# Kernel optimization log

Hardware: AMD Instinct MI355X
Metric: run time of the kernel (lower is better)

Reference implementation:

```python
import jax, jax.numpy as jnp
import numpy as np

B, N, D = 2048, 16384, 16
SIGMA0 = 0.1
LOG2PI = float(np.log(2.0 * np.pi))


def setup_inputs() -> dict:
    key = jax.random.key(0)
    k1, k2 = jax.random.split(key)
    x = jax.random.normal(k1, (B, D), dtype=jnp.float32)
    mu = jax.random.normal(k2, (N, D), dtype=jnp.float32)
    # from_sigma == log (to_sigma == exp): sigmatilde = log(sigma0)
    sigmatilde = jnp.full((N,), np.log(SIGMA0), dtype=jnp.float32)
    weights = jnp.full((N,), 1.0 / N, dtype=jnp.float32)
    return {"x": x, "mu": mu, "sigmatilde": sigmatilde, "weights": weights}


def reference(x, mu, sigmatilde, weights):
    # sigma per kernel, shape [N]
    sigma = jnp.exp(sigmatilde)
    # squared euclidean distance ||x - mu||^2 via gemm form, shape [B, N]
    sq = (
        jnp.sum(x * x, axis=1, keepdims=True)
        + jnp.sum(mu * mu, axis=1)[None, :]
        - 2.0 * (x @ mu.T)
    )
    log_det = 2.0 * D * jnp.log(sigma)  # [N]
    exponent = -0.5 * (sq / (sigma * sigma)[None, :] + log_det[None, :] + D * LOG2PI)
    exponent = exponent + jnp.log(weights)[None, :]
    # log-likelihood per sample, shape [B]
    return jax.scipy.special.logsumexp(exponent, axis=1)
```

## Files before the change

### kernel.cpp

```cpp
#include <hip/hip_runtime.h>
#include <hip/hip_bf16.h>
#include <math.h>

#define BB 2048
#define NN 16384
#define KAUG 32
#define RSA 40
#define RSX 32
#define NSLICES 128
#define CHUNKS 8
#define BT 2
#define LN2 0.6931471805599453f
#define LOG2E 1.4426950408889634f
#define LN2PI 1.8378770664093453f

typedef __attribute__((ext_vector_type(8))) short bf16x8;
typedef __attribute__((ext_vector_type(4))) float f32x4;

__device__ __forceinline__ float EXP2(float v) { return __builtin_amdgcn_exp2f(v); }

__device__ __forceinline__ unsigned pack_bf2(float a, float b) {
    __hip_bfloat162 h = __float22bfloat162_rn(make_float2(a, b));
    union { __hip_bfloat162 h2; unsigned u; } cvt;
    cvt.h2 = h;
    return cvt.u;
}
__device__ __forceinline__ float lo16f(unsigned u) { return __uint_as_float(u << 16); }
__device__ __forceinline__ float hi16f(unsigned u) { return __uint_as_float(u & 0xFFFF0000u); }

__global__ __launch_bounds__(256, 4) void kde_main(
    const float* __restrict__ x, const float* __restrict__ mu,
    const float* __restrict__ sigt, const float* __restrict__ wt,
    float2* __restrict__ part)
{
    __shared__ ushort AhL[128 * RSA], AlL[128 * RSA];
    __shared__ ushort XhL[128 * RSX], XlL[128 * RSX];

    const int tid   = threadIdx.x;
    const int slice = blockIdx.x >> 4;
    const int bgrp  = blockIdx.x & 15;

    {
        float v[KAUG];
        #pragma unroll
        for (int k = 18; k < KAUG; ++k) v[k] = 0.f;
        ushort *dh, *dl;
        if (tid < 128) {
            int n = slice * 128 + tid;
            const float4* m4 = (const float4*)(mu + (size_t)n * 16);
            float4 a = m4[0], b = m4[1], c = m4[2], d = m4[3];
            float r[16];
            *(float4*)(r + 0) = a; *(float4*)(r + 4) = b;
            *(float4*)(r + 8) = c; *(float4*)(r + 12) = d;
            float musq = 0.f;
            #pragma unroll
            for (int k = 0; k < 16; ++k) musq = fmaf(r[k], r[k], musq);
            float stv = sigt[n], wv = wt[n];
            float A2 = -0.5f * LOG2E * EXP2(-2.0f * LOG2E * stv);
            float C2 = -LOG2E * (16.f * stv + 8.f * LN2PI) + __log2f(wv);
            #pragma unroll
            for (int k = 0; k < 16; ++k) v[k] = A2 * (-2.f * r[k]);
            v[16] = fmaf(A2, musq, C2);
            v[17] = A2;
            dh = AhL + tid * RSA;
            dl = AlL + tid * RSA;
        } else {
            int b = bgrp * 128 + (tid - 128);
            const float4* x4 = (const float4*)(x + (size_t)b * 16);
            float4 a = x4[0], bb = x4[1], c = x4[2], d = x4[3];
            float r[16];
            *(float4*)(r + 0) = a;  *(float4*)(r + 4) = bb;
            *(float4*)(r + 8) = c;  *(float4*)(r + 12) = d;
            float xsq = 0.f;
            #pragma unroll
            for (int k = 0; k < 16; ++k) { v[k] = r[k]; xsq = fmaf(r[k], r[k], xsq); }
            v[16] = 1.0f;
            v[17] = xsq;
            dh = XhL + (tid - 128) * RSX;
            dl = XlL + (tid - 128) * RSX;
        }
        unsigned uh[16], ul[16];
        #pragma unroll
        for (int k = 0; k < 16; ++k) {
            unsigned h = pack_bf2(v[2*k], v[2*k+1]);
            unsigned l = pack_bf2(v[2*k]   - lo16f(h),
                                  v[2*k+1] - hi16f(h));
            uh[k] = h;  ul[k] = l;
        }
        uint4* ph = (uint4*)dh;
        uint4* pl = (uint4*)dl;
        #pragma unroll
        for (int k = 0; k < 4; ++k) {
            ph[k] = make_uint4(uh[4*k], uh[4*k+1], uh[4*k+2], uh[4*k+3]);
            pl[k] = make_uint4(ul[4*k], ul[4*k+1], ul[4*k+2], ul[4*k+3]);
        }
    }
    __syncthreads();

    const int lane = tid & 63;
    const int wv   = tid >> 6;
    const int l15  = lane & 15, g = lane >> 4;

    bf16x8 bh[BT], bl[BT];
    #pragma unroll
    for (int bt = 0; bt < BT; ++bt) {
        int xr = wv * 32 + bt * 16 + l15;
        bh[bt] = *(const bf16x8*)(XhL + xr * RSX + g * 8);
        bl[bt] = *(const bf16x8*)(XlL + xr * RSX + g * 8);
    }

    float M0 = -INFINITY, M1 = -INFINITY;
    #pragma unroll 2
    for (int c = 0; c < CHUNKS; ++c) {
        int ar = c * 16 + l15;
        bf16x8 ah = *(const bf16x8*)(AhL + ar * RSA + g * 8);
        bf16x8 al = *(const bf16x8*)(AlL + ar * RSA + g * 8);
        {
            f32x4 acc = {0.f, 0.f, 0.f, 0.f};
            acc = __builtin_amdgcn_mfma_f32_16x16x32_bf16(al, bh[0], acc, 0, 0, 0);
            acc = __builtin_amdgcn_mfma_f32_16x16x32_bf16(ah, bl[0], acc, 0, 0, 0);
            acc = __builtin_amdgcn_mfma_f32_16x16x32_bf16(ah, bh[0], acc, 0, 0, 0);
            M0 = fmaxf(M0, fmaxf(fmaxf(acc[0], acc[1]), fmaxf(acc[2], acc[3])));
        }
        {
            f32x4 acc = {0.f, 0.f, 0.f, 0.f};
            acc = __builtin_amdgcn_mfma_f32_16x16x32_bf16(al, bh[1], acc, 0, 0, 0);
            acc = __builtin_amdgcn_mfma_f32_16x16x32_bf16(ah, bl[1], acc, 0, 0, 0);
            acc = __builtin_amdgcn_mfma_f32_16x16x32_bf16(ah, bh[1], acc, 0, 0, 0);
            M1 = fmaxf(M1, fmaxf(fmaxf(acc[0], acc[1]), fmaxf(acc[2], acc[3])));
        }
    }
    M0 = fmaxf(M0, __shfl_xor(M0, 16, 64));
    M0 = fmaxf(M0, __shfl_xor(M0, 32, 64));
    M1 = fmaxf(M1, __shfl_xor(M1, 16, 64));
    M1 = fmaxf(M1, __shfl_xor(M1, 32, 64));

    asm volatile("" ::: "memory");

    float S0 = 0.f, S1 = 0.f;
    #pragma unroll 2
    for (int c = 0; c < CHUNKS; ++c) {
        int ar = c * 16 + l15;
        bf16x8 ah = *(const bf16x8*)(AhL + ar * RSA + g * 8);
        bf16x8 al = *(const bf16x8*)(AlL + ar * RSA + g * 8);
        {
            f32x4 acc = {0.f, 0.f, 0.f, 0.f};
            acc = __builtin_amdgcn_mfma_f32_16x16x32_bf16(al, bh[0], acc, 0, 0, 0);
            acc = __builtin_amdgcn_mfma_f32_16x16x32_bf16(ah, bl[0], acc, 0, 0, 0);
            acc = __builtin_amdgcn_mfma_f32_16x16x32_bf16(ah, bh[0], acc, 0, 0, 0);
            S0 += (EXP2(acc[0] - M0) + EXP2(acc[1] - M0))
                + (EXP2(acc[2] - M0) + EXP2(acc[3] - M0));
        }
        {
            f32x4 acc = {0.f, 0.f, 0.f, 0.f};
            acc = __builtin_amdgcn_mfma_f32_16x16x32_bf16(al, bh[1], acc, 0, 0, 0);
            acc = __builtin_amdgcn_mfma_f32_16x16x32_bf16(ah, bl[1], acc, 0, 0, 0);
            acc = __builtin_amdgcn_mfma_f32_16x16x32_bf16(ah, bh[1], acc, 0, 0, 0);
            S1 += (EXP2(acc[0] - M1) + EXP2(acc[1] - M1))
                + (EXP2(acc[2] - M1) + EXP2(acc[3] - M1));
        }
    }
    S0 += __shfl_xor(S0, 16, 64);
    S0 += __shfl_xor(S0, 32, 64);
    S1 += __shfl_xor(S1, 16, 64);
    S1 += __shfl_xor(S1, 32, 64);

    if (lane < 16) {
        int b0 = bgrp * 128 + wv * 32 + lane;
        part[(size_t)slice * BB + b0]      = make_float2(M0, S0);
        part[(size_t)slice * BB + b0 + 16] = make_float2(M1, S1);
    }
}

__global__ __launch_bounds__(256) void kde_reduce(
    const float2* __restrict__ part, float* __restrict__ out)
{
    int b = blockIdx.x * 256 + threadIdx.x;
    float mm[4], ss[4];
    #pragma unroll
    for (int j = 0; j < 4; ++j) { mm[j] = -INFINITY; ss[j] = 0.f; }
    #pragma unroll 4
    for (int k = 0; k < 32; ++k) {
        #pragma unroll
        for (int j = 0; j < 4; ++j) {
            float2 vv = part[(size_t)(k * 4 + j) * BB + b];
            float mn = fmaxf(mm[j], vv.x);
            ss[j] = fmaf(ss[j], EXP2(mm[j] - mn), vv.y * EXP2(vv.x - mn));
            mm[j] = mn;
        }
    }
    float mA = fmaxf(fmaxf(mm[0], mm[1]), fmaxf(mm[2], mm[3]));
    float sA = ss[0] * EXP2(mm[0] - mA) + ss[1] * EXP2(mm[1] - mA)
             + ss[2] * EXP2(mm[2] - mA) + ss[3] * EXP2(mm[3] - mA);
    out[b] = (mA + __log2f(sA)) * LN2;
}

extern "C" void kernel_launch(void* const* d_in, const int* in_sizes, int n_in,
                              void* d_out, int out_size, void* d_ws, size_t ws_size,
                              hipStream_t stream) {
    const float* x  = (const float*)d_in[0];
    const float* mu = (const float*)d_in[1];
    const float* st = (const float*)d_in[2];
    const float* w  = (const float*)d_in[3];
    float* out = (float*)d_out;

    float2* part = (float2*)d_ws;

    hipLaunchKernelGGL(kde_main, dim3(NSLICES * 16), dim3(256), 0, stream,
                       x, mu, st, w, part);
    hipLaunchKernelGGL(kde_reduce, dim3(BB / 256), dim3(256), 0, stream,
                       part, out);
}
```

Baseline: 24.39 us.

## Split logsumexp into max pass and margin-pruned exp gather pass

The main kernel now runs only the max pass. It records per-slice and per-chunk maxima, combines the global per-sample max with an atomicMax on order-preserving keys, and writes the bf16 hi/lo operands out to global memory. A second kernel recomputes dot products and exponentials only for chunks whose max lies within a 40 (log2-unit) margin of the global max, so negligible terms skip the second MFMA and exp pass. In exchange it adds a memset, several MB of chunk-max writes, atomics and global operand reloads. Accuracy relies on the dropped terms being below fp32 resolution.

```diff
diff --git a/kernel.cpp b/kernel.cpp
--- a/kernel.cpp
+++ b/kernel.cpp
@@ -9,7 +9,7 @@
 #define RSX 32
 #define NSLICES 128
 #define CHUNKS 8
-#define BT 2
+#define MARGIN 40.0f
 #define LN2 0.6931471805599453f
 #define LOG2E 1.4426950408889634f
 #define LN2PI 1.8378770664093453f
@@ -28,10 +28,22 @@
 __device__ __forceinline__ float lo16f(unsigned u) { return __uint_as_float(u << 16); }
 __device__ __forceinline__ float hi16f(unsigned u) { return __uint_as_float(u & 0xFFFF0000u); }
 
-__global__ __launch_bounds__(256, 4) void kde_main(
+__device__ __forceinline__ unsigned fkey(float f) {
+    unsigned u = __float_as_uint(f);
+    return u ^ (unsigned)(((int)u >> 31) | 0x80000000);
+}
+__device__ __forceinline__ float funkey(unsigned k) {
+    unsigned u = (k & 0x80000000u) ? (k & 0x7FFFFFFFu) : ~k;
+    return __uint_as_float(u);
+}
+
+__global__ __launch_bounds__(256, 4) void kde_max(
     const float* __restrict__ x, const float* __restrict__ mu,
     const float* __restrict__ sigt, const float* __restrict__ wt,
-    float2* __restrict__ part)
+    ushort* __restrict__ Aph, ushort* __restrict__ Apl,
+    ushort* __restrict__ Xph, ushort* __restrict__ Xpl,
+    float* __restrict__ slicemax, float* __restrict__ chunkmax,
+    unsigned* __restrict__ gkey)
 {
     __shared__ ushort AhL[128 * RSA], AlL[128 * RSA];
     __shared__ ushort XhL[128 * RSX], XlL[128 * RSX];
@@ -44,7 +56,7 @@
         float v[KAUG];
         #pragma unroll
         for (int k = 18; k < KAUG; ++k) v[k] = 0.f;
-        ushort *dh, *dl;
+        ushort *dh, *dl, *eh = nullptr, *el = nullptr;
         if (tid < 128) {
             int n = slice * 128 + tid;
             const float4* m4 = (const float4*)(mu + (size_t)n * 16);
@@ -55,15 +67,16 @@
             float musq = 0.f;
             #pragma unroll
             for (int k = 0; k < 16; ++k) musq = fmaf(r[k], r[k], musq);
-            float stv = sigt[n], wv = wt[n];
+            float stv = sigt[n], wv2 = wt[n];
             float A2 = -0.5f * LOG2E * EXP2(-2.0f * LOG2E * stv);
-            float C2 = -LOG2E * (16.f * stv + 8.f * LN2PI) + __log2f(wv);
+            float C2 = -LOG2E * (16.f * stv + 8.f * LN2PI) + __log2f(wv2);
             #pragma unroll
             for (int k = 0; k < 16; ++k) v[k] = A2 * (-2.f * r[k]);
             v[16] = fmaf(A2, musq, C2);
             v[17] = A2;
             dh = AhL + tid * RSA;
             dl = AlL + tid * RSA;
+            if (bgrp == 0) { eh = Aph + (size_t)n * KAUG; el = Apl + (size_t)n * KAUG; }
         } else {
             int b = bgrp * 128 + (tid - 128);
             const float4* x4 = (const float4*)(x + (size_t)b * 16);
@@ -78,6 +91,7 @@
             v[17] = xsq;
             dh = XhL + (tid - 128) * RSX;
             dl = XlL + (tid - 128) * RSX;
+            if (slice == 0) { eh = Xph + (size_t)b * KAUG; el = Xpl + (size_t)b * KAUG; }
         }
         unsigned uh[16], ul[16];
         #pragma unroll
@@ -91,8 +105,10 @@
         uint4* pl = (uint4*)dl;
         #pragma unroll
         for (int k = 0; k < 4; ++k) {
-            ph[k] = make_uint4(uh[4*k], uh[4*k+1], uh[4*k+2], uh[4*k+3]);
-            pl[k] = make_uint4(ul[4*k], ul[4*k+1], ul[4*k+2], ul[4*k+3]);
+            uint4 H = make_uint4(uh[4*k], uh[4*k+1], uh[4*k+2], uh[4*k+3]);
+            uint4 L = make_uint4(ul[4*k], ul[4*k+1], ul[4*k+2], ul[4*k+3]);
+            ph[k] = H;  pl[k] = L;
+            if (eh) { ((uint4*)eh)[k] = H; ((uint4*)el)[k] = L; }
         }
     }
     __syncthreads();
@@ -100,10 +116,11 @@
     const int lane = tid & 63;
     const int wv   = tid >> 6;
     const int l15  = lane & 15, g = lane >> 4;
-
-    bf16x8 bh[BT], bl[BT];
+    const int b0   = bgrp * 128 + wv * 32 + l15;
+
+    bf16x8 bh[2], bl[2];
     #pragma unroll
-    for (int bt = 0; bt < BT; ++bt) {
+    for (int bt = 0; bt < 2; ++bt) {
         int xr = wv * 32 + bt * 16 + l15;
         bh[bt] = *(const bf16x8*)(XhL + xr * RSX + g * 8);
         bl[bt] = *(const bf16x8*)(XlL + xr * RSX + g * 8);
@@ -115,84 +132,83 @@
         int ar = c * 16 + l15;
         bf16x8 ah = *(const bf16x8*)(AhL + ar * RSA + g * 8);
         bf16x8 al = *(const bf16x8*)(AlL + ar * RSA + g * 8);
-        {
+        f32x4 a0 = {0.f, 0.f, 0.f, 0.f};
+        a0 = __builtin_amdgcn_mfma_f32_16x16x32_bf16(al, bh[0], a0, 0, 0, 0);
+        a0 = __builtin_amdgcn_mfma_f32_16x16x32_bf16(ah, bl[0], a0, 0, 0, 0);
+        a0 = __builtin_amdgcn_mfma_f32_16x16x32_bf16(ah, bh[0], a0, 0, 0, 0);
+        float cm0 = fmaxf(fmaxf(a0[0], a0[1]), fmaxf(a0[2], a0[3]));
+        cm0 = fmaxf(cm0, __shfl_xor(cm0, 16, 64));
+        cm0 = fmaxf(cm0, __shfl_xor(cm0, 32, 64));
+        f32x4 a1 = {0.f, 0.f, 0.f, 0.f};
+        a1 = __builtin_amdgcn_mfma_f32_16x16x32_bf16(al, bh[1], a1, 0, 0, 0);
+        a1 = __builtin_amdgcn_mfma_f32_16x16x32_bf16(ah, bl[1], a1, 0, 0, 0);
+        a1 = __builtin_amdgcn_mfma_f32_16x16x32_bf16(ah, bh[1], a1, 0, 0, 0);
+        float cm1 = fmaxf(fmaxf(a1[0], a1[1]), fmaxf(a1[2], a1[3]));
+        cm1 = fmaxf(cm1, __shfl_xor(cm1, 16, 64));
+        cm1 = fmaxf(cm1, __shfl_xor(cm1, 32, 64));
+        if (lane < 16) {
+            chunkmax[(size_t)(slice * 8 + c) * BB + b0]      = cm0;
+            chunkmax[(size_t)(slice * 8 + c) * BB + b0 + 16] = cm1;
+        }
+        M0 = fmaxf(M0, cm0);
+        M1 = fmaxf(M1, cm1);
+    }
+
+    if (lane < 16) {
+        slicemax[(size_t)slice * BB + b0]      = M0;
+        slicemax[(size_t)slice * BB + b0 + 16] = M1;
+        unsigned k0 = fkey(M0);
+        if (k0 > gkey[b0])      atomicMax(&gkey[b0], k0);
+        unsigned k1 = fkey(M1);
+        if (k1 > gkey[b0 + 16]) atomicMax(&gkey[b0 + 16], k1);
+    }
+}
+
+__global__ __launch_bounds__(256) void kde_gather(
+    const ushort* __restrict__ Aph, const ushort* __restrict__ Apl,
+    const ushort* __restrict__ Xph, const ushort* __restrict__ Xpl,
+    const float* __restrict__ slicemax, const float* __restrict__ chunkmax,
+    const unsigned* __restrict__ gkey, float* __restrict__ out)
+{
+    __shared__ float sS[4][16];
+    const int tid  = threadIdx.x;
+    const int lane = tid & 63;
+    const int wv   = tid >> 6;
+    const int l15  = lane & 15, g = lane >> 4;
+    const int b    = blockIdx.x * 16 + l15;
+
+    const float M = funkey(gkey[b]);
+    bf16x8 bh = *(const bf16x8*)(Xph + (size_t)b * KAUG + g * 8);
+    bf16x8 bl = *(const bf16x8*)(Xpl + (size_t)b * KAUG + g * 8);
+
+    float S = 0.f;
+    for (int sl = wv; sl < NSLICES; sl += 4) {
+        float sm = slicemax[(size_t)sl * BB + b];
+        if (!__any(sm >= M - MARGIN)) continue;
+        #pragma unroll
+        for (int c = 0; c < CHUNKS; ++c) {
+            float cm = chunkmax[(size_t)(sl * 8 + c) * BB + b];
+            if (!__any(cm >= M - MARGIN)) continue;
+            int n = sl * 128 + c * 16 + l15;
+            bf16x8 ah = *(const bf16x8*)(Aph + (size_t)n * KAUG + g * 8);
+            bf16x8 al = *(const bf16x8*)(Apl + (size_t)n * KAUG + g * 8);
             f32x4 acc = {0.f, 0.f, 0.f, 0.f};
-            acc = __builtin_amdgcn_mfma_f32_16x16x32_bf16(al, bh[0], acc, 0, 0, 0);
-            acc = __builtin_amdgcn_mfma_f32_16x16x32_bf16(ah, bl[0], acc, 0, 0, 0);
-            acc = __builtin_amdgcn_mfma_f32_16x16x32_bf16(ah, bh[0], acc, 0, 0, 0);
-            M0 = fmaxf(M0, fmaxf(fmaxf(acc[0], acc[1]), fmaxf(acc[2], acc[3])));
-        }
-        {
-            f32x4 acc = {0.f, 0.f, 0.f, 0.f};
-            acc = __builtin_amdgcn_mfma_f32_16x16x32_bf16(al, bh[1], acc, 0, 0, 0);
-            acc = __builtin_amdgcn_mfma_f32_16x16x32_bf16(ah, bl[1], acc, 0, 0, 0);
-            acc = __builtin_amdgcn_mfma_f32_16x16x32_bf16(ah, bh[1], acc, 0, 0, 0);
-            M1 = fmaxf(M1, fmaxf(fmaxf(acc[0], acc[1]), fmaxf(acc[2], acc[3])));
-        }
-    }
-    M0 = fmaxf(M0, __shfl_xor(M0, 16, 64));
-    M0 = fmaxf(M0, __shfl_xor(M0, 32, 64));
-    M1 = fmaxf(M1, __shfl_xor(M1, 16, 64));
-    M1 = fmaxf(M1, __shfl_xor(M1, 32, 64));
-
-    asm volatile("" ::: "memory");
-
-    float S0 = 0.f, S1 = 0.f;
-    #pragma unroll 2
-    for (int c = 0; c < CHUNKS; ++c) {
-        int ar = c * 16 + l15;
-        bf16x8 ah = *(const bf16x8*)(AhL + ar * RSA + g * 8);
-        bf16x8 al = *(const bf16x8*)(AlL + ar * RSA + g * 8);
-        {
-            f32x4 acc = {0.f, 0.f, 0.f, 0.f};
-            acc = __builtin_amdgcn_mfma_f32_16x16x32_bf16(al, bh[0], acc, 0, 0, 0);
-            acc = __builtin_amdgcn_mfma_f32_16x16x32_bf16(ah, bl[0], acc, 0, 0, 0);
-            acc = __builtin_amdgcn_mfma_f32_16x16x32_bf16(ah, bh[0], acc, 0, 0, 0);
-            S0 += (EXP2(acc[0] - M0) + EXP2(acc[1] - M0))
-                + (EXP2(acc[2] - M0) + EXP2(acc[3] - M0));
-        }
-        {
-            f32x4 acc = {0.f, 0.f, 0.f, 0.f};
-            acc = __builtin_amdgcn_mfma_f32_16x16x32_bf16(al, bh[1], acc, 0, 0, 0);
-            acc = __builtin_amdgcn_mfma_f32_16x16x32_bf16(ah, bl[1], acc, 0, 0, 0);
-            acc = __builtin_amdgcn_mfma_f32_16x16x32_bf16(ah, bh[1], acc, 0, 0, 0);
-            S1 += (EXP2(acc[0] - M1) + EXP2(acc[1] - M1))
-                + (EXP2(acc[2] - M1) + EXP2(acc[3] - M1));
-        }
-    }
-    S0 += __shfl_xor(S0, 16, 64);
-    S0 += __shfl_xor(S0, 32, 64);
-    S1 += __shfl_xor(S1, 16, 64);
-    S1 += __shfl_xor(S1, 32, 64);
-
-    if (lane < 16) {
-        int b0 = bgrp * 128 + wv * 32 + lane;
-        part[(size_t)slice * BB + b0]      = make_float2(M0, S0);
-        part[(size_t)slice * BB + b0 + 16] = make_float2(M1, S1);
-    }
-}
-
-__global__ __launch_bounds__(256) void kde_reduce(
-    const float2* __restrict__ part, float* __restrict__ out)
-{
-    int b = blockIdx.x * 256 + threadIdx.x;
-    float mm[4], ss[4];
-    #pragma unroll
-    for (int j = 0; j < 4; ++j) { mm[j] = -INFINITY; ss[j] = 0.f; }
-    #pragma unroll 4
-    for (int k = 0; k < 32; ++k) {
-        #pragma unroll
-        for (int j = 0; j < 4; ++j) {
-            float2 vv = part[(size_t)(k * 4 + j) * BB + b];
-            float mn = fmaxf(mm[j], vv.x);
-            ss[j] = fmaf(ss[j], EXP2(mm[j] - mn), vv.y * EXP2(vv.x - mn));
-            mm[j] = mn;
-        }
-    }
-    float mA = fmaxf(fmaxf(mm[0], mm[1]), fmaxf(mm[2], mm[3]));
-    float sA = ss[0] * EXP2(mm[0] - mA) + ss[1] * EXP2(mm[1] - mA)
-             + ss[2] * EXP2(mm[2] - mA) + ss[3] * EXP2(mm[3] - mA);
-    out[b] = (mA + __log2f(sA)) * LN2;
+            acc = __builtin_amdgcn_mfma_f32_16x16x32_bf16(al, bh, acc, 0, 0, 0);
+            acc = __builtin_amdgcn_mfma_f32_16x16x32_bf16(ah, bl, acc, 0, 0, 0);
+            acc = __builtin_amdgcn_mfma_f32_16x16x32_bf16(ah, bh, acc, 0, 0, 0);
+            S += (EXP2(acc[0] - M) + EXP2(acc[1] - M))
+               + (EXP2(acc[2] - M) + EXP2(acc[3] - M));
+        }
+    }
+    S += __shfl_xor(S, 16, 64);
+    S += __shfl_xor(S, 32, 64);
+    if (lane < 16) sS[wv][l15] = S;
+    __syncthreads();
+    if (tid < 16) {
+        float St = (sS[0][tid] + sS[1][tid]) + (sS[2][tid] + sS[3][tid]);
+        int bb = blockIdx.x * 16 + tid;
+        out[bb] = (funkey(gkey[bb]) + __log2f(St)) * LN2;
+    }
 }
 
 extern "C" void kernel_launch(void* const* d_in, const int* in_sizes, int n_in,
@@ -204,10 +220,19 @@
     const float* w  = (const float*)d_in[3];
     float* out = (float*)d_out;
 
-    float2* part = (float2*)d_ws;
-
-    hipLaunchKernelGGL(kde_main, dim3(NSLICES * 16), dim3(256), 0, stream,
-                       x, mu, st, w, part);
-    hipLaunchKernelGGL(kde_reduce, dim3(BB / 256), dim3(256), 0, stream,
-                       part, out);
-}
+    char* ws = (char*)d_ws;
+    unsigned* gkey   = (unsigned*)ws;
+    float* slicemax  = (float*)(ws + 8192);
+    float* chunkmax  = (float*)(ws + 8192 + (1u << 20));
+    ushort* Aph      = (ushort*)(ws + 8192 + (9u << 20));
+    ushort* Apl      = (ushort*)(ws + 8192 + (10u << 20));
+    ushort* Xph      = (ushort*)(ws + 8192 + (11u << 20));
+    ushort* Xpl      = (ushort*)(ws + 8192 + (11u << 20) + (128u << 10));
+
+    hipMemsetAsync(gkey, 0, BB * sizeof(unsigned), stream);
+
+    hipLaunchKernelGGL(kde_max, dim3(NSLICES * 16), dim3(256), 0, stream,
+                       x, mu, st, w, Aph, Apl, Xph, Xpl, slicemax, chunkmax, gkey);
+    hipLaunchKernelGGL(kde_gather, dim3(BB / 16), dim3(256), 0, stream,
+                       Aph, Apl, Xph, Xpl, slicemax, chunkmax, gkey, out);
+}
```

After: 91.53 us. 275% more time.
